# Performance work log

Measured on AMD Instinct MI355X. Metric: run time of the kernel, lower is better.

The kernel has to match this reference:

```python
import jax, jax.numpy as jnp
import numpy as np

N_NODES = 50000
N_EDGES = 600000
D = 128        # input_dim == hidden_dim
OUT = 2        # output_dim
N_LAYERS = 6


def setup_inputs() -> dict:
    key = jax.random.key(0)
    ks = jax.random.split(key, 6)
    scale = 1.0 / np.sqrt(D)
    x = jax.random.normal(ks[0], (N_NODES, D), jnp.float32)
    edge_index = jax.random.randint(ks[1], (2, N_EDGES), 0, N_NODES)
    Wl = jax.random.normal(ks[2], (N_LAYERS, D, D), jnp.float32) * scale  # neighbor (lin_l) weights
    Wr = jax.random.normal(ks[3], (N_LAYERS, D, D), jnp.float32) * scale  # root (lin_r) weights
    bl = jnp.zeros((N_LAYERS, D), jnp.float32)                            # lin_l bias
    fc_W = jax.random.normal(ks[4], (D, OUT), jnp.float32) * scale
    fc_b = jnp.zeros((OUT,), jnp.float32)
    return {"x": x, "edge_index": edge_index, "Wl": Wl, "Wr": Wr, "bl": bl,
            "fc_W": fc_W, "fc_b": fc_b}


def _sage_conv(h, src, dst, deg_inv, Wl_i, Wr_i, bl_i):
    # mean aggregation over incoming edges: gather -> scatter-add -> normalize
    agg = jax.ops.segment_sum(h[src], dst, num_segments=h.shape[0]) * deg_inv  # [N, D]
    return agg @ Wl_i + h @ Wr_i + bl_i


def reference(x, edge_index, Wl, Wr, bl, fc_W, fc_b):
    src, dst = edge_index[0], edge_index[1]
    deg = jax.ops.segment_sum(jnp.ones(src.shape, x.dtype), dst, num_segments=x.shape[0])
    deg_inv = (1.0 / jnp.maximum(deg, 1.0))[:, None]  # [N, 1]
    h = x
    # ReLU follows every SAGEConv: inner act of each GraphSAGE block + explicit F.relu after each block
    for i in range(N_LAYERS):
        h = _sage_conv(h, src, dst, deg_inv, Wl[i], Wr[i], bl[i])
        h = jax.nn.relu(h)
    return h @ fc_W + fc_b  # [N, OUT]
```

## Files before the change

kernel.cpp:

```cpp
#include <hip/hip_runtime.h>
#include <hip/hip_bf16.h>

#define N_NODES 50000
#define N_EDGES 600000
#define DD 128
#define N_LAYERS 6
#define SCAN_BLOCKS 196
#define N_CHUNKS 3125

typedef __attribute__((ext_vector_type(8))) short bf16x8;
typedef __attribute__((ext_vector_type(4))) float floatx4;

__device__ __forceinline__ void ldsdma16(const void* g, void* l) {
    __builtin_amdgcn_global_load_lds(
        (const __attribute__((address_space(1))) char*)g,
        (__attribute__((address_space(3))) char*)l, 16, 0, 0);
}

__device__ __forceinline__ unsigned short f2b(float f) {
    unsigned u = __float_as_uint(f);
    unsigned r = (u + 0x7FFFu + ((u >> 16) & 1u)) >> 16;
    return (unsigned short)r;
}


__global__ void zero_counts(int* __restrict__ deg, int* __restrict__ cursor) {
    int i = blockIdx.x * blockDim.x + threadIdx.x;
    if (i < N_NODES) { deg[i] = 0; cursor[i] = 0; }
}

__global__ void count_deg(const int* __restrict__ dst, int* __restrict__ deg) {
    int e = blockIdx.x * blockDim.x + threadIdx.x;
    if (e < N_EDGES) atomicAdd(&deg[dst[e]], 1);
}

__global__ void block_sums(const int* __restrict__ deg, int* __restrict__ bsum) {
    __shared__ int s[256];
    int tid = threadIdx.x;
    int i = blockIdx.x * 256 + tid;
    int v = (i < N_NODES) ? deg[i] : 0;
    s[tid] = v;
    __syncthreads();
    #pragma unroll
    for (int off = 128; off > 0; off >>= 1) {
        if (tid < off) s[tid] += s[tid + off];
        __syncthreads();
    }
    if (tid == 0) bsum[blockIdx.x] = s[0];
}

__global__ void scan_bsums(int* __restrict__ bsum, int* __restrict__ offsets) {
    __shared__ int s[256];
    int tid = threadIdx.x;
    int v = (tid < SCAN_BLOCKS) ? bsum[tid] : 0;
    s[tid] = v;
    __syncthreads();
    for (int off = 1; off < 256; off <<= 1) {
        int t = (tid >= off) ? s[tid - off] : 0;
        __syncthreads();
        s[tid] += t;
        __syncthreads();
    }
    if (tid < SCAN_BLOCKS) bsum[tid] = s[tid] - v;
    if (tid == 0) offsets[N_NODES] = N_EDGES;
}

__global__ void write_offsets(const int* __restrict__ deg, const int* __restrict__ bsum,
                              int* __restrict__ offsets, float* __restrict__ deg_inv) {
    __shared__ int s[256];
    int tid = threadIdx.x;
    int i = blockIdx.x * 256 + tid;
    int v = (i < N_NODES) ? deg[i] : 0;
    s[tid] = v;
    __syncthreads();
    for (int off = 1; off < 256; off <<= 1) {
        int t = (tid >= off) ? s[tid - off] : 0;
        __syncthreads();
        s[tid] += t;
        __syncthreads();
    }
    if (i < N_NODES) {
        offsets[i] = bsum[blockIdx.x] + s[tid] - v;
        deg_inv[i] = 1.0f / (float)(v > 1 ? v : 1);
    }
}

__global__ void fill_csr(const int* __restrict__ src, const int* __restrict__ dst,
                         const int* __restrict__ offsets, int* __restrict__ cursor,
                         int* __restrict__ csr_src) {
    int e = blockIdx.x * blockDim.x + threadIdx.x;
    if (e < N_EDGES) {
        int d = dst[e];
        int p = atomicAdd(&cursor[d], 1);
        csr_src[offsets[d] + p] = src[e];
    }
}


__global__ void x_to_bf16(const float* __restrict__ x, unsigned short* __restrict__ hx) {
    int idx = blockIdx.x * blockDim.x + threadIdx.x;
    int b = idx * 4;
    float4 v = *(const float4*)(x + b);
    ushort4 o;
    o.x = f2b(v.x); o.y = f2b(v.y); o.z = f2b(v.z); o.w = f2b(v.w);
    *(ushort4*)(hx + b) = o;
}

__global__ void prep_weights(const float* __restrict__ Wl, const float* __restrict__ Wr,
                             unsigned short* __restrict__ WT2) {
    int idx = blockIdx.x * blockDim.x + threadIdx.x;
    int l   = idx >> 15;
    int rem = idx & 32767;
    int n   = rem >> 8;
    int k2  = rem & 255;
    const float* W = (k2 < 128 ? Wl : Wr) + (size_t)l * DD * DD + (size_t)(k2 & 127) * DD + n;
    WT2[idx] = f2b(*W);
}


__global__ void aggregate(const unsigned short* __restrict__ hin, const int* __restrict__ offsets,
                          const int* __restrict__ csr_src, const float* __restrict__ deg_inv,
                          unsigned short* __restrict__ agg) {
    int wid  = threadIdx.x >> 6;
    int lane = threadIdx.x & 63;
    int grp  = lane >> 4;
    int l16  = lane & 15;
    int node = blockIdx.x * 4 + wid;
    if (node >= N_NODES) return;
    int s = offsets[node], e = offsets[node + 1];

    float a0=0,a1=0,a2=0,a3=0,a4=0,a5=0,a6=0,a7=0;
    for (int j = s + grp; j < e; j += 4) {
        int src = csr_src[j];
        uint4 v = *(const uint4*)(hin + (size_t)src * DD + l16 * 8);
        a0 += __uint_as_float(v.x << 16); a1 += __uint_as_float(v.x & 0xFFFF0000u);
        a2 += __uint_as_float(v.y << 16); a3 += __uint_as_float(v.y & 0xFFFF0000u);
        a4 += __uint_as_float(v.z << 16); a5 += __uint_as_float(v.z & 0xFFFF0000u);
        a6 += __uint_as_float(v.w << 16); a7 += __uint_as_float(v.w & 0xFFFF0000u);
    }
    a0 += __shfl_xor(a0, 16, 64); a1 += __shfl_xor(a1, 16, 64);
    a2 += __shfl_xor(a2, 16, 64); a3 += __shfl_xor(a3, 16, 64);
    a4 += __shfl_xor(a4, 16, 64); a5 += __shfl_xor(a5, 16, 64);
    a6 += __shfl_xor(a6, 16, 64); a7 += __shfl_xor(a7, 16, 64);
    a0 += __shfl_xor(a0, 32, 64); a1 += __shfl_xor(a1, 32, 64);
    a2 += __shfl_xor(a2, 32, 64); a3 += __shfl_xor(a3, 32, 64);
    a4 += __shfl_xor(a4, 32, 64); a5 += __shfl_xor(a5, 32, 64);
    a6 += __shfl_xor(a6, 32, 64); a7 += __shfl_xor(a7, 32, 64);

    if (grp == 0) {
        float di = deg_inv[node];
        uint4 o;
        o.x = (unsigned)f2b(a0 * di) | ((unsigned)f2b(a1 * di) << 16);
        o.y = (unsigned)f2b(a2 * di) | ((unsigned)f2b(a3 * di) << 16);
        o.z = (unsigned)f2b(a4 * di) | ((unsigned)f2b(a5 * di) << 16);
        o.w = (unsigned)f2b(a6 * di) | ((unsigned)f2b(a7 * di) << 16);
        *(uint4*)(agg + (size_t)node * DD + l16 * 8) = o;
    }
}


__launch_bounds__(512, 2)
__global__ void gemm_resW(const unsigned short* __restrict__ Agg,
                          const unsigned short* __restrict__ H,
                          const unsigned short* __restrict__ WT2,
                          const float* __restrict__ bias,
                          unsigned short* __restrict__ Cout) {
    __shared__ __align__(16) unsigned short sW[128 * 256];
    __shared__ __align__(16) unsigned short sA[8][4096];

    int tid  = threadIdx.x;
    int wid  = tid >> 6, lane = tid & 63;
    int l15  = lane & 15, q = lane >> 4;

    for (int t = tid; t < 4096; t += 512) {
        int col = t >> 5, c = t & 31;
        uint4 v = *(const uint4*)(WT2 + (size_t)col * 256 + c * 8);
        *(uint4*)(sW + ((size_t)col * 32 + (c ^ (col & 7))) * 8) = v;
    }
    __syncthreads();

    float bcol[8];
    #pragma unroll
    for (int j = 0; j < 8; ++j) bcol[j] = bias[j * 16 + l15];

    unsigned short* myA = &sA[wid][0];

    for (int chunk = blockIdx.x * 8 + wid; chunk < N_CHUNKS; chunk += 2048) {
        int row0 = chunk * 16;
        #pragma unroll
        for (int i = 0; i < 4; ++i) {
            int r  = i * 4 + q;
            int cg = l15 ^ (r & 7);
            ldsdma16(Agg + (size_t)(row0 + r) * DD + cg * 8, myA + (size_t)i * 512 + lane * 8);
        }
        #pragma unroll
        for (int i = 0; i < 4; ++i) {
            int r  = i * 4 + q;
            int cg = l15 ^ (r & 7);
            ldsdma16(H + (size_t)(row0 + r) * DD + cg * 8, myA + 2048 + (size_t)i * 512 + lane * 8);
        }
        __builtin_amdgcn_s_waitcnt(0);

        floatx4 acc[8];
        #pragma unroll
        for (int j = 0; j < 8; ++j) acc[j] = (floatx4){0.f, 0.f, 0.f, 0.f};

        #pragma unroll
        for (int s = 0; s < 8; ++s) {
            int cglob = s * 4 + q;
            int reg   = cglob >> 4;
            int cin   = cglob & 15;
            bf16x8 aF = *(const bf16x8*)(myA + (size_t)reg * 2048 +
                                         ((size_t)l15 * 16 + (cin ^ (l15 & 7))) * 8);
            #pragma unroll
            for (int j = 0; j < 8; ++j) {
                int col = j * 16 + l15;
                bf16x8 bF = *(const bf16x8*)(sW + ((size_t)col * 32 + (cglob ^ (col & 7))) * 8);
                acc[j] = __builtin_amdgcn_mfma_f32_16x16x32_bf16(aF, bF, acc[j], 0, 0, 0);
            }
        }

        #pragma unroll
        for (int r = 0; r < 4; ++r) {
            int row = row0 + q * 4 + r;
            #pragma unroll
            for (int j = 0; j < 8; ++j) {
                float v = acc[j][r] + bcol[j];
                Cout[(size_t)row * DD + j * 16 + l15] = f2b(fmaxf(v, 0.f));
            }
        }
    }
}


__global__ void fc_kernel(const unsigned short* __restrict__ h, const float* __restrict__ fcW,
                          const float* __restrict__ fcb, float* __restrict__ out) {
    int n = blockIdx.x * blockDim.x + threadIdx.x;
    if (n >= N_NODES) return;
    const unsigned* hr = (const unsigned*)(h + (size_t)n * DD);
    float s0 = fcb[0], s1 = fcb[1];
    #pragma unroll 8
    for (int k = 0; k < 64; ++k) {
        unsigned v = hr[k];
        float h0 = __uint_as_float(v << 16);
        float h1 = __uint_as_float(v & 0xFFFF0000u);
        s0 += h0 * fcW[(2 * k) * 2]     + h1 * fcW[(2 * k + 1) * 2];
        s1 += h0 * fcW[(2 * k) * 2 + 1] + h1 * fcW[(2 * k + 1) * 2 + 1];
    }
    out[n * 2] = s0; out[n * 2 + 1] = s1;
}


extern "C" void kernel_launch(void* const* d_in, const int* in_sizes, int n_in,
                              void* d_out, int out_size, void* d_ws, size_t ws_size,
                              hipStream_t stream) {
    const float* x    = (const float*)d_in[0];
    const int*   ei   = (const int*)d_in[1];
    const float* Wl   = (const float*)d_in[2];
    const float* Wr   = (const float*)d_in[3];
    const float* bl   = (const float*)d_in[4];
    const float* fcW  = (const float*)d_in[5];
    const float* fcb  = (const float*)d_in[6];
    float* out = (float*)d_out;

    const int* srcIdx = ei;
    const int* dstIdx = ei + N_EDGES;

    char* ws = (char*)d_ws;
    size_t off = 0;
    auto bump = [&](size_t bytes) { char* p = ws + off; off = (off + bytes + 255) & ~(size_t)255; return p; };
    int*   deg     = (int*)  bump(N_NODES * 4);
    int*   cursor  = (int*)  bump(N_NODES * 4);
    int*   offsets = (int*)  bump((N_NODES + 1) * 4);
    int*   bsum    = (int*)  bump(SCAN_BLOCKS * 4);
    float* deg_inv = (float*)bump(N_NODES * 4);
    int*   csr     = (int*)  bump(N_EDGES * 4);
    unsigned short* hx   = (unsigned short*)bump((size_t)N_NODES * DD * 2);
    unsigned short* hb0  = (unsigned short*)bump((size_t)N_NODES * DD * 2);
    unsigned short* hb1  = (unsigned short*)bump((size_t)N_NODES * DD * 2);
    unsigned short* agg  = (unsigned short*)bump((size_t)N_NODES * DD * 2);
    unsigned short* WT2  = (unsigned short*)bump((size_t)N_LAYERS * 128 * 256 * 2);
    (void)ws_size;

    zero_counts<<<(N_NODES + 255) / 256, 256, 0, stream>>>(deg, cursor);
    count_deg<<<(N_EDGES + 255) / 256, 256, 0, stream>>>(dstIdx, deg);
    block_sums<<<SCAN_BLOCKS, 256, 0, stream>>>(deg, bsum);
    scan_bsums<<<1, 256, 0, stream>>>(bsum, offsets);
    write_offsets<<<SCAN_BLOCKS, 256, 0, stream>>>(deg, bsum, offsets, deg_inv);
    fill_csr<<<(N_EDGES + 255) / 256, 256, 0, stream>>>(srcIdx, dstIdx, offsets, cursor, csr);
    x_to_bf16<<<(N_NODES * DD / 4 + 255) / 256, 256, 0, stream>>>(x, hx);
    prep_weights<<<(N_LAYERS * 128 * 256 + 255) / 256, 256, 0, stream>>>(Wl, Wr, WT2);

    const unsigned short* hin = hx;
    unsigned short* hbuf[2] = { hb0, hb1 };
    for (int l = 0; l < N_LAYERS; ++l) {
        aggregate<<<(N_NODES + 3) / 4, 256, 0, stream>>>(hin, offsets, csr, deg_inv, agg);
        unsigned short* hout = hbuf[l & 1];
        gemm_resW<<<256, 512, 0, stream>>>(
            agg, hin, WT2 + (size_t)l * 128 * 256, bl + (size_t)l * DD, hout);
        hin = hout;
    }
    fc_kernel<<<(N_NODES + 255) / 256, 256, 0, stream>>>(hin, fcW, fcb, out);
}
```

Baseline: 401.7 us.

## Fuse prep kernels, fold final FC into last GEMM, remap blocks across XCDs

Merges the zeroing, x-to-bf16 conversion and weight-prep kernels into one launch. Fuses the final 128x2 FC projection into the last layer's GEMM epilogue via a cross-lane shuffle reduction, which skips writing and rereading the last hidden state. Also remaps block indices in both aggregate and GEMM so that consecutive node groups land on the same XCD, aiming at better L2 locality. The remap pads aggregate to 12512 blocks and relies on guards for the out-of-range nodes.

```diff
diff --git a/kernel.cpp b/kernel.cpp
--- a/kernel.cpp
+++ b/kernel.cpp
@@ -8,6 +8,11 @@
 #define SCAN_BLOCKS 196
 #define N_CHUNKS 3125
 
+#define XB16_T 1600000
+#define ZERO_T 50000
+#define PREPW_T 196608
+#define PREP_TOTAL (XB16_T + ZERO_T + PREPW_T)
+
 typedef __attribute__((ext_vector_type(8))) short bf16x8;
 typedef __attribute__((ext_vector_type(4))) float floatx4;
 
@@ -24,10 +29,31 @@
 }
 
 
-__global__ void zero_counts(int* __restrict__ deg, int* __restrict__ cursor) {
-    int i = blockIdx.x * blockDim.x + threadIdx.x;
-    if (i < N_NODES) { deg[i] = 0; cursor[i] = 0; }
-}
+__global__ void prep_all(const float* __restrict__ x, unsigned short* __restrict__ hx,
+                         const float* __restrict__ Wl, const float* __restrict__ Wr,
+                         unsigned short* __restrict__ WT2,
+                         int* __restrict__ deg, int* __restrict__ cursor) {
+    int gid = blockIdx.x * blockDim.x + threadIdx.x;
+    if (gid < XB16_T) {
+        int b = gid * 4;
+        float4 v = *(const float4*)(x + b);
+        ushort4 o;
+        o.x = f2b(v.x); o.y = f2b(v.y); o.z = f2b(v.z); o.w = f2b(v.w);
+        *(ushort4*)(hx + b) = o;
+    } else if (gid < XB16_T + ZERO_T) {
+        int i = gid - XB16_T;
+        deg[i] = 0; cursor[i] = 0;
+    } else if (gid < PREP_TOTAL) {
+        int idx = gid - (XB16_T + ZERO_T);
+        int l   = idx >> 15;
+        int rem = idx & 32767;
+        int n   = rem >> 8;
+        int k2  = rem & 255;
+        const float* W = (k2 < 128 ? Wl : Wr) + (size_t)l * DD * DD + (size_t)(k2 & 127) * DD + n;
+        WT2[idx] = f2b(*W);
+    }
+}
+
 
 __global__ void count_deg(const int* __restrict__ dst, int* __restrict__ deg) {
     int e = blockIdx.x * blockDim.x + threadIdx.x;
@@ -97,27 +123,6 @@
 }
 
 
-__global__ void x_to_bf16(const float* __restrict__ x, unsigned short* __restrict__ hx) {
-    int idx = blockIdx.x * blockDim.x + threadIdx.x;
-    int b = idx * 4;
-    float4 v = *(const float4*)(x + b);
-    ushort4 o;
-    o.x = f2b(v.x); o.y = f2b(v.y); o.z = f2b(v.z); o.w = f2b(v.w);
-    *(ushort4*)(hx + b) = o;
-}
-
-__global__ void prep_weights(const float* __restrict__ Wl, const float* __restrict__ Wr,
-                             unsigned short* __restrict__ WT2) {
-    int idx = blockIdx.x * blockDim.x + threadIdx.x;
-    int l   = idx >> 15;
-    int rem = idx & 32767;
-    int n   = rem >> 8;
-    int k2  = rem & 255;
-    const float* W = (k2 < 128 ? Wl : Wr) + (size_t)l * DD * DD + (size_t)(k2 & 127) * DD + n;
-    WT2[idx] = f2b(*W);
-}
-
-
 __global__ void aggregate(const unsigned short* __restrict__ hin, const int* __restrict__ offsets,
                           const int* __restrict__ csr_src, const float* __restrict__ deg_inv,
                           unsigned short* __restrict__ agg) {
@@ -125,12 +130,15 @@
     int lane = threadIdx.x & 63;
     int grp  = lane >> 4;
     int l16  = lane & 15;
-    int node = blockIdx.x * 4 + wid;
+    int b = blockIdx.x;
+    int x = b & 7, s = b >> 3;
+    int group = 4 * (x + 8 * (s >> 2)) + (s & 3);
+    int node = group * 4 + wid;
     if (node >= N_NODES) return;
-    int s = offsets[node], e = offsets[node + 1];
+    int s0 = offsets[node], e0 = offsets[node + 1];
 
     float a0=0,a1=0,a2=0,a3=0,a4=0,a5=0,a6=0,a7=0;
-    for (int j = s + grp; j < e; j += 4) {
+    for (int j = s0 + grp; j < e0; j += 4) {
         int src = csr_src[j];
         uint4 v = *(const uint4*)(hin + (size_t)src * DD + l16 * 8);
         a0 += __uint_as_float(v.x << 16); a1 += __uint_as_float(v.x & 0xFFFF0000u);
@@ -164,7 +172,11 @@
                           const unsigned short* __restrict__ H,
                           const unsigned short* __restrict__ WT2,
                           const float* __restrict__ bias,
-                          unsigned short* __restrict__ Cout) {
+                          unsigned short* __restrict__ Cout,
+                          const float* __restrict__ fcW,
+                          const float* __restrict__ fcb,
+                          float* __restrict__ out,
+                          int doFC) {
     __shared__ __align__(16) unsigned short sW[128 * 256];
     __shared__ __align__(16) unsigned short sA[8][4096];
 
@@ -183,9 +195,18 @@
     #pragma unroll
     for (int j = 0; j < 8; ++j) bcol[j] = bias[j * 16 + l15];
 
+    float2 fcw[8];
+    float fb0 = 0.f, fb1 = 0.f;
+    if (doFC) {
+        #pragma unroll
+        for (int j = 0; j < 8; ++j) fcw[j] = *(const float2*)(fcW + (j * 16 + l15) * 2);
+        fb0 = fcb[0]; fb1 = fcb[1];
+    }
+
     unsigned short* myA = &sA[wid][0];
-
-    for (int chunk = blockIdx.x * 8 + wid; chunk < N_CHUNKS; chunk += 2048) {
+    int x = blockIdx.x & 7, bb = blockIdx.x >> 3;
+
+    for (int chunk = x + 8 * (bb * 8 + wid); chunk < N_CHUNKS; chunk += 2048) {
         int row0 = chunk * 16;
         #pragma unroll
         for (int i = 0; i < 4; ++i) {
@@ -220,34 +241,38 @@
             }
         }
 
-        #pragma unroll
-        for (int r = 0; r < 4; ++r) {
-            int row = row0 + q * 4 + r;
+        if (!doFC) {
             #pragma unroll
-            for (int j = 0; j < 8; ++j) {
-                float v = acc[j][r] + bcol[j];
-                Cout[(size_t)row * DD + j * 16 + l15] = f2b(fmaxf(v, 0.f));
+            for (int r = 0; r < 4; ++r) {
+                int row = row0 + q * 4 + r;
+                #pragma unroll
+                for (int j = 0; j < 8; ++j) {
+                    float v = acc[j][r] + bcol[j];
+                    Cout[(size_t)row * DD + j * 16 + l15] = f2b(fmaxf(v, 0.f));
+                }
+            }
+        } else {
+            #pragma unroll
+            for (int r = 0; r < 4; ++r) {
+                float p0 = 0.f, p1 = 0.f;
+                #pragma unroll
+                for (int j = 0; j < 8; ++j) {
+                    float v = fmaxf(acc[j][r] + bcol[j], 0.f);
+                    p0 += v * fcw[j].x;
+                    p1 += v * fcw[j].y;
+                }
+                p0 += __shfl_xor(p0, 1, 64); p1 += __shfl_xor(p1, 1, 64);
+                p0 += __shfl_xor(p0, 2, 64); p1 += __shfl_xor(p1, 2, 64);
+                p0 += __shfl_xor(p0, 4, 64); p1 += __shfl_xor(p1, 4, 64);
+                p0 += __shfl_xor(p0, 8, 64); p1 += __shfl_xor(p1, 8, 64);
+                if (l15 == 0) {
+                    int row = row0 + q * 4 + r;
+                    out[row * 2]     = p0 + fb0;
+                    out[row * 2 + 1] = p1 + fb1;
+                }
             }
         }
     }
-}
-
-
-__global__ void fc_kernel(const unsigned short* __restrict__ h, const float* __restrict__ fcW,
-                          const float* __restrict__ fcb, float* __restrict__ out) {
-    int n = blockIdx.x * blockDim.x + threadIdx.x;
-    if (n >= N_NODES) return;
-    const unsigned* hr = (const unsigned*)(h + (size_t)n * DD);
-    float s0 = fcb[0], s1 = fcb[1];
-    #pragma unroll 8
-    for (int k = 0; k < 64; ++k) {
-        unsigned v = hr[k];
-        float h0 = __uint_as_float(v << 16);
-        float h1 = __uint_as_float(v & 0xFFFF0000u);
-        s0 += h0 * fcW[(2 * k) * 2]     + h1 * fcW[(2 * k + 1) * 2];
-        s1 += h0 * fcW[(2 * k) * 2 + 1] + h1 * fcW[(2 * k + 1) * 2 + 1];
-    }
-    out[n * 2] = s0; out[n * 2 + 1] = s1;
 }
 
 
@@ -282,23 +307,22 @@
     unsigned short* WT2  = (unsigned short*)bump((size_t)N_LAYERS * 128 * 256 * 2);
     (void)ws_size;
 
-    zero_counts<<<(N_NODES + 255) / 256, 256, 0, stream>>>(deg, cursor);
+    prep_all<<<(PREP_TOTAL + 255) / 256, 256, 0, stream>>>(x, hx, Wl, Wr, WT2, deg, cursor);
     count_deg<<<(N_EDGES + 255) / 256, 256, 0, stream>>>(dstIdx, deg);
     block_sums<<<SCAN_BLOCKS, 256, 0, stream>>>(deg, bsum);
     scan_bsums<<<1, 256, 0, stream>>>(bsum, offsets);
     write_offsets<<<SCAN_BLOCKS, 256, 0, stream>>>(deg, bsum, offsets, deg_inv);
     fill_csr<<<(N_EDGES + 255) / 256, 256, 0, stream>>>(srcIdx, dstIdx, offsets, cursor, csr);
-    x_to_bf16<<<(N_NODES * DD / 4 + 255) / 256, 256, 0, stream>>>(x, hx);
-    prep_weights<<<(N_LAYERS * 128 * 256 + 255) / 256, 256, 0, stream>>>(Wl, Wr, WT2);
 
     const unsigned short* hin = hx;
     unsigned short* hbuf[2] = { hb0, hb1 };
     for (int l = 0; l < N_LAYERS; ++l) {
-        aggregate<<<(N_NODES + 3) / 4, 256, 0, stream>>>(hin, offsets, csr, deg_inv, agg);
+        int last = (l == N_LAYERS - 1);
+        aggregate<<<12512, 256, 0, stream>>>(hin, offsets, csr, deg_inv, agg);
         unsigned short* hout = hbuf[l & 1];
         gemm_resW<<<256, 512, 0, stream>>>(
-            agg, hin, WT2 + (size_t)l * 128 * 256, bl + (size_t)l * DD, hout);
+            agg, hin, WT2 + (size_t)l * 128 * 256, bl + (size_t)l * DD, hout,
+            fcW, fcb, out, last);
         hin = hout;
     }
-    fc_kernel<<<(N_NODES + 255) / 256, 256, 0, stream>>>(hin, fcW, fcb, out);
-}
+}
```

After: 392.7 us. 2.2% less time.
